# Optimization experiments

Measured on AMD Instinct MI355X. Metric: run time of the kernel, lower is better.

## Reference

```python
import jax, jax.numpy as jnp
import numpy as np

B, C, D, H = 16, 64, 512, 8
SEQ_LEN, LABEL_LEN, PRED_LEN = 1024, 512, 512
DEC_LEN = LABEL_LEN + PRED_LEN
DFF, KSIZE, FACTOR = 2048, 25, 3
E_LAYERS, D_LAYERS = 2, 1


def _pos_emb(L, d):
    pos = np.arange(L, dtype=np.float32)[:, None]
    div = np.exp(np.arange(0, d, 2, dtype=np.float32) * (-np.log(10000.0) / d))
    pe = np.zeros((L, d), np.float32)
    pe[:, 0::2] = np.sin(pos * div)
    pe[:, 1::2] = np.cos(pos * div)
    return jnp.asarray(pe)


def moving_mean(x, k=KSIZE):
    # AvgPool1d(k, stride=1) with replicate padding of (k-1)//2 at both ends
    pad = (k - 1) // 2
    xp = jnp.concatenate([jnp.repeat(x[:, :1], pad, 1), x, jnp.repeat(x[:, -1:], pad, 1)], axis=1)
    cs = jnp.cumsum(xp, axis=1)
    cs = jnp.concatenate([jnp.zeros_like(cs[:, :1]), cs], axis=1)
    return (cs[:, k:] - cs[:, :-k]) / k


def series_decomp(x):
    mm = moving_mean(x)
    return x - mm, mm


def circ_conv3(x, W):
    # Conv1d kernel=3, circular padding=1, no bias. x [B,L,Cin], W [3,Cin,Cout]
    L = x.shape[1]
    xp = jnp.concatenate([x[:, -1:], x, x[:, :1]], axis=1)
    return sum(jnp.einsum('blc,cd->bld', xp[:, k:k + L], W[k]) for k in range(3))


def my_layernorm(x, g, b):
    # LayerNorm then subtract per-sample mean over the time axis (special seasonal layernorm)
    mu = x.mean(-1, keepdims=True)
    var = x.var(-1, keepdims=True)
    xh = (x - mu) / jnp.sqrt(var + 1e-5) * g + b
    return xh - xh.mean(axis=1, keepdims=True)


def autocorrelation(q, k, v):
    # q,k,v: [B,L,H,E]. FFT cross-correlation, top-k lag selection, time-delay aggregation.
    L = q.shape[1]
    qf = jnp.fft.rfft(q.transpose(0, 2, 3, 1), axis=-1)
    kf = jnp.fft.rfft(k.transpose(0, 2, 3, 1), axis=-1)
    corr = jnp.fft.irfft(qf * jnp.conj(kf), n=L, axis=-1)  # [B,H,E,L]
    top_k = int(FACTOR * np.log(L))
    w, delay = jax.lax.top_k(corr.mean(axis=(1, 2)), top_k)  # [B,K]
    tc = jax.nn.softmax(w, axis=-1)
    vp = v.transpose(0, 2, 3, 1)  # [B,H,E,L]
    base = jnp.arange(L)
    agg = jnp.zeros_like(vp)
    for i in range(top_k):  # small fixed K (= int(factor*log L) = 20)
        idx = (base[None, :] + delay[:, i:i + 1]) % L  # circular shift == gather on doubled values
        pattern = jnp.take_along_axis(vp, idx[:, None, None, :], axis=-1)
        agg = agg + pattern * tc[:, i][:, None, None, None]
    return agg.transpose(0, 3, 1, 2)  # [B,L,H,E]


def ac_layer(q_in, kv_in, Wq, bq, Wk, bk, Wv, bv, Wo, bo):
    Bb, L, _ = q_in.shape
    S = kv_in.shape[1]
    E = D // H
    q = (q_in @ Wq + bq).reshape(Bb, L, H, E)
    k = (kv_in @ Wk + bk).reshape(Bb, S, H, E)
    v = (kv_in @ Wv + bv).reshape(Bb, S, H, E)
    out = autocorrelation(q, k, v)  # L == S by construction here
    return out.reshape(Bb, L, D) @ Wo + bo


def _forward(x_enc, x_dec, enc_emb_w, dec_emb_w, enc_Wq, enc_bq, enc_Wk, enc_bk, enc_Wv, enc_bv, enc_Wo, enc_bo, enc_ff1, enc_ff2, enc_ng, enc_nb, dsa_Wq, dsa_bq, dsa_Wk, dsa_bk, dsa_Wv, dsa_bv, dsa_Wo, dsa_bo, dca_Wq, dca_bq, dca_Wk, dca_bk, dca_Wv, dca_bv, dca_Wo, dca_bo, dec_ff1, dec_ff2, dec_trend_w, proj_w, proj_b):
    mean = jnp.repeat(x_enc.mean(axis=1, keepdims=True), PRED_LEN, axis=1)
    zeros = jnp.zeros((x_dec.shape[0], PRED_LEN, x_dec.shape[2]), x_enc.dtype)
    seasonal_init, trend_init = series_decomp(x_enc)
    trend = jnp.concatenate([trend_init[:, -LABEL_LEN:], mean], axis=1)
    seasonal_init = jnp.concatenate([seasonal_init[:, -LABEL_LEN:], zeros], axis=1)
    # encoder (DataEmbedding_wo_temp = token circular conv + sinusoidal pos, dropout=0)
    x = circ_conv3(x_enc, enc_emb_w) + _pos_emb(SEQ_LEN, D)[None]
    for l in range(E_LAYERS):
        x = x + ac_layer(x, x, enc_Wq[l], enc_bq[l], enc_Wk[l], enc_bk[l], enc_Wv[l], enc_bv[l], enc_Wo[l], enc_bo[l])
        x, _ = series_decomp(x)
        y = jax.nn.gelu(x @ enc_ff1[l], approximate=False) @ enc_ff2[l]
        x, _ = series_decomp(x + y)
    enc_out = my_layernorm(x, enc_ng, enc_nb)
    # decoder
    xd = circ_conv3(seasonal_init, dec_emb_w) + _pos_emb(DEC_LEN, D)[None]
    for l in range(D_LAYERS):
        xd = xd + ac_layer(xd, xd, dsa_Wq[l], dsa_bq[l], dsa_Wk[l], dsa_bk[l], dsa_Wv[l], dsa_bv[l], dsa_Wo[l], dsa_bo[l])
        xd, t1 = series_decomp(xd)
        xd = xd + ac_layer(xd, enc_out, dca_Wq[l], dca_bq[l], dca_Wk[l], dca_bk[l], dca_Wv[l], dca_bv[l], dca_Wo[l], dca_bo[l])
        xd, t2 = series_decomp(xd)
        y = jax.nn.gelu(xd @ dec_ff1[l], approximate=False) @ dec_ff2[l]
        xd, t3 = series_decomp(xd + y)
        trend = trend + circ_conv3(t1 + t2 + t3, dec_trend_w[l])  # trend projection conv
    seasonal = xd @ proj_w + proj_b
    out = trend + seasonal
    return out[:, -PRED_LEN:]


def setup_inputs():
    key = jax.random.key(0)
    ks = iter(jax.random.split(key, 64))
    def n(shape, s=0.02):
        return jax.random.normal(next(ks), shape, jnp.float32) * s
    inp = {}
    inp['x_enc'] = jax.random.normal(next(ks), (B, SEQ_LEN, C), jnp.float32)
    inp['x_dec'] = jax.random.normal(next(ks), (B, DEC_LEN, C), jnp.float32)
    inp['enc_emb_w'] = n((3, C, D))
    inp['dec_emb_w'] = n((3, C, D))
    for p in ['Wq', 'Wk', 'Wv', 'Wo']:
        bp = p.replace('W', 'b')
        inp['enc_' + p] = n((E_LAYERS, D, D)); inp['enc_' + bp] = jnp.zeros((E_LAYERS, D))
        inp['dsa_' + p] = n((D_LAYERS, D, D)); inp['dsa_' + bp] = jnp.zeros((D_LAYERS, D))
        inp['dca_' + p] = n((D_LAYERS, D, D)); inp['dca_' + bp] = jnp.zeros((D_LAYERS, D))
    inp['enc_ff1'] = n((E_LAYERS, D, DFF)); inp['enc_ff2'] = n((E_LAYERS, DFF, D))
    inp['enc_ng'] = jnp.ones((D,), jnp.float32); inp['enc_nb'] = jnp.zeros((D,), jnp.float32)
    inp['dec_ff1'] = n((D_LAYERS, D, DFF)); inp['dec_ff2'] = n((D_LAYERS, DFF, D))
    inp['dec_trend_w'] = n((D_LAYERS, 3, D, C))
    inp['proj_w'] = n((D, C)); inp['proj_b'] = jnp.zeros((C,), jnp.float32)
    return inp


def reference(x_enc, x_dec, enc_emb_w, dec_emb_w, enc_Wq, enc_bq, enc_Wk, enc_bk, enc_Wv, enc_bv, enc_Wo, enc_bo, enc_ff1, enc_ff2, enc_ng, enc_nb, dsa_Wq, dsa_bq, dsa_Wk, dsa_bk, dsa_Wv, dsa_bv, dsa_Wo, dsa_bo, dca_Wq, dca_bq, dca_Wk, dca_bk, dca_Wv, dca_bv, dca_Wo, dca_bo, dec_ff1, dec_ff2, dec_trend_w, proj_w, proj_b):
    return _forward(x_enc, x_dec, enc_emb_w, dec_emb_w, enc_Wq, enc_bq, enc_Wk, enc_bk, enc_Wv, enc_bv, enc_Wo, enc_bo, enc_ff1, enc_ff2, enc_ng, enc_nb, dsa_Wq, dsa_bq, dsa_Wk, dsa_bk, dsa_Wv, dsa_bv, dsa_Wo, dsa_bo, dca_Wq, dca_bq, dca_Wk, dca_bk, dca_Wv, dca_bv, dca_Wo, dca_bo, dec_ff1, dec_ff2, dec_trend_w, proj_w, proj_b)
```

## Files before the change

kernel.cpp:

```cpp
#include <hip/hip_runtime.h>
#include <math.h>

#define B_   16
#define L_   1024
#define C_   64
#define D_   512
#define DFF_ 2048
#define TOPK_ 20

typedef float f4 __attribute__((ext_vector_type(4)));
typedef float f32x4 __attribute__((ext_vector_type(4)));
typedef short bf16x8 __attribute__((ext_vector_type(8)));
typedef unsigned short u16x8 __attribute__((ext_vector_type(8)));

__device__ __forceinline__ unsigned short f2bf(float f) {
    union { float f; unsigned u; } a; a.f = f;
    unsigned r = a.u + 0x7fff + ((a.u >> 16) & 1);
    return (unsigned short)(r >> 16);
}
__device__ __forceinline__ float bf2f(unsigned short h) {
    union { unsigned u; float f; } a; a.u = ((unsigned)h) << 16;
    return a.f;
}

__device__ __forceinline__ float gelu_fast(float c) {
    float z  = c * 0.70710678118654752f;
    float az = fabsf(z);
    float t  = __builtin_amdgcn_rcpf(fmaf(0.3275911f, az, 1.0f));
    float p  = fmaf(fmaf(fmaf(fmaf(1.061405429f, t, -1.453152027f), t,
                              1.421413741f), t, -0.284496736f), t, 0.254829592f) * t;
    float e  = __expf(-z * z);
    float ea = fmaf(-p, e, 1.0f);
    float er = copysignf(ea, z);
    return 0.5f * c * (1.0f + er);
}

__device__ __forceinline__ void gld16(const void* g, void* l) {
    __builtin_amdgcn_global_load_lds(
        (const __attribute__((address_space(1))) unsigned int*)g,
        (__attribute__((address_space(3))) unsigned int*)l, 16, 0, 0);
}


__global__ __launch_bounds__(256)
void gemm_bf16(const unsigned short* __restrict__ A, const unsigned short* __restrict__ Bt,
               float* __restrict__ Cf, unsigned short* __restrict__ Cb,
               unsigned short* __restrict__ Cl,
               const float* __restrict__ bias, int M, int N, int K, int flags, int nx)
{
    __shared__ unsigned short As0[128 * 32], As1[128 * 32];
    __shared__ unsigned short Bs0[128 * 32], Bs1[128 * 32];
    const int tid = threadIdx.x;
    const int wave = tid >> 6, lane = tid & 63;

    int total = gridDim.x;
    int h = blockIdx.x;
    int lidx = h;
    if ((total & 7) == 0) {
        int q = total >> 3;
        lidx = (h & 7) * q + (h >> 3);
    }
    const int bm = (lidx / nx) * 128, bn = (lidx % nx) * 128;
    const int wm = (wave >> 1) << 6, wn = (wave & 1) << 6;

    const int r0 = (wave << 5) + (lane >> 2);
    const int kq = (((lane & 3) ^ ((lane >> 3) & 3)) << 3);
    const unsigned short* Ap0 = A + (size_t)(bm + r0) * K + kq;
    const unsigned short* Ap1 = Ap0 + (size_t)16 * K;
    const unsigned short* Bp0 = Bt + (size_t)(bn + r0) * K + kq;
    const unsigned short* Bp1 = Bp0 + (size_t)16 * K;
    const int wo0 = (wave << 5) * 32, wo1 = ((wave << 5) + 16) * 32;

    const int la = lane & 15, h4 = lane >> 4;
    const int sw = (la >> 1) & 3;
    f32x4 acc[4][4] = {};

    for (int k0 = 0; k0 < K; k0 += 64) {
        gld16(Ap0 + k0, &As0[wo0]);      gld16(Ap1 + k0, &As0[wo1]);
        gld16(Bp0 + k0, &Bs0[wo0]);      gld16(Bp1 + k0, &Bs0[wo1]);
        gld16(Ap0 + k0 + 32, &As1[wo0]); gld16(Ap1 + k0 + 32, &As1[wo1]);
        gld16(Bp0 + k0 + 32, &Bs1[wo0]); gld16(Bp1 + k0 + 32, &Bs1[wo1]);
        __syncthreads();
        bf16x8 a[4], b[4];
#pragma unroll
        for (int i = 0; i < 4; ++i) {
            a[i] = *(const bf16x8*)&As0[(wm + i * 16 + la) * 32 + ((h4 ^ sw) << 3)];
            b[i] = *(const bf16x8*)&Bs0[(wn + i * 16 + la) * 32 + ((h4 ^ sw) << 3)];
        }
#pragma unroll
        for (int mi = 0; mi < 4; ++mi)
#pragma unroll
            for (int ni = 0; ni < 4; ++ni)
                acc[mi][ni] = __builtin_amdgcn_mfma_f32_16x16x32_bf16(a[mi], b[ni], acc[mi][ni], 0, 0, 0);
#pragma unroll
        for (int i = 0; i < 4; ++i) {
            a[i] = *(const bf16x8*)&As1[(wm + i * 16 + la) * 32 + ((h4 ^ sw) << 3)];
            b[i] = *(const bf16x8*)&Bs1[(wn + i * 16 + la) * 32 + ((h4 ^ sw) << 3)];
        }
#pragma unroll
        for (int mi = 0; mi < 4; ++mi)
#pragma unroll
            for (int ni = 0; ni < 4; ++ni)
                acc[mi][ni] = __builtin_amdgcn_mfma_f32_16x16x32_bf16(a[mi], b[ni], acc[mi][ni], 0, 0, 0);
        __syncthreads();
    }

#pragma unroll
    for (int mi = 0; mi < 4; ++mi) {
#pragma unroll
        for (int r = 0; r < 4; ++r) {
            int m = bm + wm + mi * 16 + h4 * 4 + r;
#pragma unroll
            for (int ni = 0; ni < 4; ++ni) {
                int n = bn + wn + ni * 16 + la;
                float c = acc[mi][ni][r];
                if (bias) c += bias[n];
                if (flags & 2) c = gelu_fast(c);
                size_t o = (size_t)m * N + n;
                if (Cf) { if (flags & 1) Cf[o] += c; else Cf[o] = c; }
                if (Cb) {
                    unsigned short hb = f2bf(c);
                    Cb[o] = hb;
                    if (Cl) Cl[o] = f2bf(c - bf2f(hb));
                }
            }
        }
    }
}

__global__ __launch_bounds__(512)
void gemm256_gelu(const unsigned short* __restrict__ A, const unsigned short* __restrict__ Bt,
                  unsigned short* __restrict__ Cb, int M, int N, int K, int nx)
{
    __shared__ unsigned short As[2][16384];
    __shared__ unsigned short Bs[2][16384];
    const int tid = threadIdx.x;
    const int wave = tid >> 6, lane = tid & 63;

    int total = gridDim.x;
    int h = blockIdx.x;
    int lidx = h;
    if ((total & 7) == 0) {
        int q = total >> 3;
        lidx = (h & 7) * q + (h >> 3);
    }
    const int bm = (lidx / nx) * 256, bn = (lidx % nx) * 256;
    const int wm = (wave >> 2) << 7, wn = (wave & 3) << 6;

    const int r0 = (wave << 5) + (lane >> 2);
    const int kq = (((lane & 3) ^ ((lane >> 3) & 3)) << 3);
    const unsigned short* Ap0 = A + (size_t)(bm + r0) * K + kq;
    const unsigned short* Ap1 = Ap0 + (size_t)16 * K;
    const unsigned short* Bp0 = Bt + (size_t)(bn + r0) * K + kq;
    const unsigned short* Bp1 = Bp0 + (size_t)16 * K;
    const int wo0 = (wave << 5) * 32, wo1 = ((wave << 5) + 16) * 32;

    const int la = lane & 15, h4 = lane >> 4;
    const int sw = (la >> 1) & 3;
    f32x4 acc[8][4] = {};

    gld16(Ap0, &As[0][wo0]);             gld16(Ap1, &As[0][wo1]);
    gld16(Bp0, &Bs[0][wo0]);             gld16(Bp1, &Bs[0][wo1]);
    gld16(Ap0 + 32, &As[0][8192 + wo0]); gld16(Ap1 + 32, &As[0][8192 + wo1]);
    gld16(Bp0 + 32, &Bs[0][8192 + wo0]); gld16(Bp1 + 32, &Bs[0][8192 + wo1]);
    __syncthreads();

    const int nt = K >> 6;
    for (int t = 0; t < nt; ++t) {
        if (t + 1 < nt) {
            const int k0 = (t + 1) << 6;
            const int nb2 = (t + 1) & 1;
            gld16(Ap0 + k0, &As[nb2][wo0]);             gld16(Ap1 + k0, &As[nb2][wo1]);
            gld16(Bp0 + k0, &Bs[nb2][wo0]);             gld16(Bp1 + k0, &Bs[nb2][wo1]);
            gld16(Ap0 + k0 + 32, &As[nb2][8192 + wo0]); gld16(Ap1 + k0 + 32, &As[nb2][8192 + wo1]);
            gld16(Bp0 + k0 + 32, &Bs[nb2][8192 + wo0]); gld16(Bp1 + k0 + 32, &Bs[nb2][8192 + wo1]);
        }
        const int cb = t & 1;
#pragma unroll
        for (int hh = 0; hh < 2; ++hh) {
            const int hb = hh << 13;
            bf16x8 a[8], b[4];
#pragma unroll
            for (int i = 0; i < 8; ++i)
                a[i] = *(const bf16x8*)&As[cb][hb + (wm + i * 16 + la) * 32 + ((h4 ^ sw) << 3)];
#pragma unroll
            for (int i = 0; i < 4; ++i)
                b[i] = *(const bf16x8*)&Bs[cb][hb + (wn + i * 16 + la) * 32 + ((h4 ^ sw) << 3)];
#pragma unroll
            for (int mi = 0; mi < 8; ++mi)
#pragma unroll
                for (int ni = 0; ni < 4; ++ni)
                    acc[mi][ni] = __builtin_amdgcn_mfma_f32_16x16x32_bf16(a[mi], b[ni], acc[mi][ni], 0, 0, 0);
        }
        __syncthreads();
    }

#pragma unroll
    for (int mi = 0; mi < 8; ++mi)
#pragma unroll
        for (int r = 0; r < 4; ++r) {
            int m = bm + wm + mi * 16 + h4 * 4 + r;
#pragma unroll
            for (int ni = 0; ni < 4; ++ni) {
                int n = bn + wn + ni * 16 + la;
                Cb[(size_t)m * N + n] = f2bf(gelu_fast(acc[mi][ni][r]));
            }
        }
}

__global__ __launch_bounds__(256)
void gemm_split(const unsigned short* __restrict__ A, const unsigned short* __restrict__ Bt,
                unsigned short* __restrict__ o0h, unsigned short* __restrict__ o0l, const float* __restrict__ b0,
                unsigned short* __restrict__ o1h, unsigned short* __restrict__ o1l, const float* __restrict__ b1,
                unsigned short* __restrict__ o2h, unsigned short* __restrict__ o2l, const float* __restrict__ b2,
                float* __restrict__ Gz, int M, int N, int K, int nx)
{
    __shared__ unsigned short As0[128 * 32], As1[128 * 32];
    __shared__ unsigned short Bs0[128 * 32], Bs1[128 * 32];
    const int tid = threadIdx.x;
    const int wave = tid >> 6, lane = tid & 63;

    int total = gridDim.x;
    int h = blockIdx.x;
    if (Gz && h < 64) Gz[h * 256 + tid] = 0.f;
    int lidx = h;
    if ((total & 7) == 0) {
        int q = total >> 3;
        lidx = (h & 7) * q + (h >> 3);
    }
    const int bm = (lidx / nx) * 128, bn = (lidx % nx) * 128;
    const int wm = (wave >> 1) << 6, wn = (wave & 1) << 6;

    const int sel = bn >> 9;
    unsigned short* oh = sel == 0 ? o0h : (sel == 1 ? o1h : o2h);
    unsigned short* ol = sel == 0 ? o0l : (sel == 1 ? o1l : o2l);
    const float* bias  = sel == 0 ? b0  : (sel == 1 ? b1  : b2);
    const int nb = bn & 511;

    const int r0 = (wave << 5) + (lane >> 2);
    const int kq = (((lane & 3) ^ ((lane >> 3) & 3)) << 3);
    const unsigned short* Ap0 = A + (size_t)(bm + r0) * K + kq;
    const unsigned short* Ap1 = Ap0 + (size_t)16 * K;
    const unsigned short* Bp0 = Bt + (size_t)(bn + r0) * K + kq;
    const unsigned short* Bp1 = Bp0 + (size_t)16 * K;
    const int wo0 = (wave << 5) * 32, wo1 = ((wave << 5) + 16) * 32;

    const int la = lane & 15, h4 = lane >> 4;
    const int sw = (la >> 1) & 3;
    f32x4 acc[4][4] = {};

    for (int k0 = 0; k0 < K; k0 += 64) {
        gld16(Ap0 + k0, &As0[wo0]);      gld16(Ap1 + k0, &As0[wo1]);
        gld16(Bp0 + k0, &Bs0[wo0]);      gld16(Bp1 + k0, &Bs0[wo1]);
        gld16(Ap0 + k0 + 32, &As1[wo0]); gld16(Ap1 + k0 + 32, &As1[wo1]);
        gld16(Bp0 + k0 + 32, &Bs1[wo0]); gld16(Bp1 + k0 + 32, &Bs1[wo1]);
        __syncthreads();
        bf16x8 a[4], b[4];
#pragma unroll
        for (int i = 0; i < 4; ++i) {
            a[i] = *(const bf16x8*)&As0[(wm + i * 16 + la) * 32 + ((h4 ^ sw) << 3)];
            b[i] = *(const bf16x8*)&Bs0[(wn + i * 16 + la) * 32 + ((h4 ^ sw) << 3)];
        }
#pragma unroll
        for (int mi = 0; mi < 4; ++mi)
#pragma unroll
            for (int ni = 0; ni < 4; ++ni)
                acc[mi][ni] = __builtin_amdgcn_mfma_f32_16x16x32_bf16(a[mi], b[ni], acc[mi][ni], 0, 0, 0);
#pragma unroll
        for (int i = 0; i < 4; ++i) {
            a[i] = *(const bf16x8*)&As1[(wm + i * 16 + la) * 32 + ((h4 ^ sw) << 3)];
            b[i] = *(const bf16x8*)&Bs1[(wn + i * 16 + la) * 32 + ((h4 ^ sw) << 3)];
        }
#pragma unroll
        for (int mi = 0; mi < 4; ++mi)
#pragma unroll
            for (int ni = 0; ni < 4; ++ni)
                acc[mi][ni] = __builtin_amdgcn_mfma_f32_16x16x32_bf16(a[mi], b[ni], acc[mi][ni], 0, 0, 0);
        __syncthreads();
    }

#pragma unroll
    for (int mi = 0; mi < 4; ++mi) {
#pragma unroll
        for (int r = 0; r < 4; ++r) {
            int m = bm + wm + mi * 16 + h4 * 4 + r;
#pragma unroll
            for (int ni = 0; ni < 4; ++ni) {
                int n2 = nb + wn + ni * 16 + la;
                float c = acc[mi][ni][r] + bias[n2];
                size_t o = (size_t)m * 512 + n2;
                unsigned short hb = f2bf(c);
                oh[o] = hb;
                if (ol) ol[o] = f2bf(c - bf2f(hb));
            }
        }
    }
}

__global__ __launch_bounds__(256)
void tcast_kernel(const float* __restrict__ W, unsigned short* __restrict__ Wt, int R, int Cc)
{
    __shared__ float t[32][33];
    int bx = blockIdx.x * 32, by = blockIdx.y * 32;
    int tx = threadIdx.x & 31, ty = threadIdx.x >> 5;
#pragma unroll
    for (int i = 0; i < 32; i += 8)
        t[ty + i][tx] = W[(size_t)(by + ty + i) * Cc + bx + tx];
    __syncthreads();
#pragma unroll
    for (int i = 0; i < 32; i += 8)
        Wt[(size_t)(bx + ty + i) * R + by + tx] = f2bf(t[tx][ty + i]);
}

struct P16 { const float* p[16]; };
__global__ __launch_bounds__(256)
void tcast_all(P16 srcs, unsigned short* __restrict__ dst)
{
    __shared__ float t[32][33];
    const float* W = srcs.p[blockIdx.z];
    unsigned short* Wt = dst + (size_t)blockIdx.z * 262144;
    int bx = blockIdx.x * 32, by = blockIdx.y * 32;
    int tx = threadIdx.x & 31, ty = threadIdx.x >> 5;
#pragma unroll
    for (int i = 0; i < 32; i += 8)
        t[ty + i][tx] = W[(size_t)(by + ty + i) * 512 + bx + tx];
    __syncthreads();
#pragma unroll
    for (int i = 0; i < 32; i += 8)
        Wt[(size_t)(bx + ty + i) * 512 + by + tx] = f2bf(t[tx][ty + i]);
}

__global__ __launch_bounds__(256)
void pegen_kernel(float* __restrict__ PE)
{
    int idx = blockIdx.x * blockDim.x + threadIdx.x;
    int n = idx & 511, l = idx >> 9;
    int i2 = n & ~1;
    float div = expf(-(float)i2 * 0.017988946039015984f);
    float ang = (float)l * div;
    PE[idx] = (n & 1) ? cosf(ang) : sinf(ang);
}

__global__ __launch_bounds__(256)
void emb_kernel(const float* __restrict__ A, const float* __restrict__ W,
                const float* __restrict__ PEt,
                float* __restrict__ Xo, unsigned short* __restrict__ Xb)
{
    __shared__ float As[66][68];
    __shared__ float Ws[3][64][64];
    const int tid = threadIdx.x;
    const int bn = blockIdx.x * 64, bm = blockIdx.y * 64;
    const int base = bm & ~1023;
    for (int i = tid; i < 66 * 64; i += 256) {
        int r = i >> 6, c = i & 63;
        int l = (bm - base) + r - 1;
        if (l < 0) l += 1024; else if (l >= 1024) l -= 1024;
        As[r][c] = A[(size_t)(base + l) * 64 + c];
    }
    for (int i = tid; i < 3 * 64 * 64; i += 256) {
        int tap = i >> 12, rem = i & 4095, k = rem >> 6, c = rem & 63;
        Ws[tap][k][c] = W[((size_t)tap * 64 + k) * 512 + bn + c];
    }
    __syncthreads();
    const int tx = tid & 15, ty = tid >> 4;
    float acc[4][4] = {};
    for (int tap = 0; tap < 3; ++tap)
        for (int k = 0; k < 64; ++k) {
            f4 bv = *(const f4*)&Ws[tap][k][tx * 4];
#pragma unroll
            for (int i = 0; i < 4; ++i) {
                float a = As[ty * 4 + i + tap][k];
#pragma unroll
                for (int j = 0; j < 4; ++j)
                    acc[i][j] = fmaf(a, bv[j], acc[i][j]);
            }
        }
#pragma unroll
    for (int i = 0; i < 4; ++i) {
        int m = bm + ty * 4 + i;
        int l = m & 1023;
#pragma unroll
        for (int j = 0; j < 4; ++j) {
            int n = bn + tx * 4 + j;
            float c = acc[i][j] + PEt[((size_t)l << 9) + n];
            size_t o = (size_t)m * 512 + n;
            Xo[o] = c;
            Xb[o] = f2bf(c);
        }
    }
}

__global__ __launch_bounds__(256)
void tail_kernel(const float* __restrict__ TSUM, const float* __restrict__ T1,
                 const float* __restrict__ Wt, const float* __restrict__ pw,
                 float* __restrict__ PC, float* __restrict__ PP)
{
    __shared__ float Ts[18][17];
    __shared__ float T1s[16][17];
    __shared__ float Ws[3][16][64];
    __shared__ float Ps[16][64];
    const int tid = threadIdx.x;
    const int bo = blockIdx.x * 16;
    const int kc = blockIdx.y;
    const int b = bo >> 9;
    const int lbase = (bo & 511) + 512;
    const size_t rowbase = (size_t)b << 10;
    const int tc4 = (tid & 15) * 4;
    const int tr = tid >> 4;
    const int kbeg = kc * 64, kend = kbeg + 64;
    float cacc[4] = {}, pacc[4] = {};

    for (int k0 = kbeg; k0 < kend; k0 += 16) {
        for (int i = tid; i < 18 * 16; i += 256) {
            int r = i >> 4, c = i & 15;
            int l = lbase + r - 1; if (l >= 1024) l -= 1024;
            Ts[r][c] = TSUM[(rowbase + l) * 512 + k0 + c];
        }
        {
            int r = tid >> 4, c = tid & 15;
            T1s[r][c] = T1[(rowbase + lbase + r) * 512 + k0 + c];
        }
        for (int i = tid; i < 3 * 16 * 16; i += 256) {
            int tap = i / 256, rem = i & 255, k = rem >> 4, c4 = (rem & 15) * 4;
            *(f4*)&Ws[tap][k][c4] = *(const f4*)&Wt[((size_t)tap * 512 + k0 + k) * 64 + c4];
        }
        if (tid < 256) {
            int k = tid >> 4, c4 = (tid & 15) * 4;
            *(f4*)&Ps[k][c4] = *(const f4*)&pw[(size_t)(k0 + k) * 64 + c4];
        }
        __syncthreads();
        for (int tap = 0; tap < 3; ++tap)
#pragma unroll
            for (int k = 0; k < 16; ++k) {
                f4 bv = *(const f4*)&Ws[tap][k][tc4];
                float a = Ts[tr + tap][k];
#pragma unroll
                for (int j = 0; j < 4; ++j)
                    cacc[j] = fmaf(a, bv[j], cacc[j]);
            }
#pragma unroll
        for (int k = 0; k < 16; ++k) {
            f4 bv = *(const f4*)&Ps[k][tc4];
            float a = T1s[tr][k];
#pragma unroll
            for (int j = 0; j < 4; ++j)
                pacc[j] = fmaf(a, bv[j], pacc[j]);
        }
        __syncthreads();
    }
    size_t o = ((size_t)kc * 8192 + (bo + tr)) * 64 + tc4;
    *(f4*)&PC[o] = *(f4*)cacc;
    *(f4*)&PP[o] = *(f4*)pacc;
}

__global__ __launch_bounds__(256)
void tailred_kernel(const float* __restrict__ PC, const float* __restrict__ PP,
                    const float* __restrict__ MEANC, const float* __restrict__ pb,
                    float* __restrict__ OUT)
{
    int idx = blockIdx.x * blockDim.x + threadIdx.x;
    int n = idx & 63;
    int b = idx >> 15;
    const size_t S = (size_t)8192 * 64;
    float cs = PC[idx];
    float ps = PP[idx];
#pragma unroll
    for (int s = 1; s < 8; ++s) {
        cs += PC[s * S + idx];
        ps += PP[s * S + idx];
    }
    OUT[idx] = (MEANC[(b << 6) + n] + cs) + (ps + pb[n]);
}

__global__ __launch_bounds__(512)
void corr_mfma(const unsigned short* __restrict__ Qh, const unsigned short* __restrict__ Ql,
               const unsigned short* __restrict__ Kh, const unsigned short* __restrict__ Kl,
               float* __restrict__ G)
{
    __shared__ unsigned short Qhs[2][8192], Qls[2][8192], Khs[2][8192], Kls[2][8192];
    __shared__ float diagw[8][512];
    const int tid = threadIdx.x;
    const int wave = tid >> 6, lane = tid & 63;

    const int i_ = blockIdx.x;
    const int x_ = i_ & 7, j_ = i_ >> 3;
    const int b = x_ + ((j_ >> 4) << 3);
    const int tile = j_ & 15;
    const int bt = (tile >> 2) * 256, bs = (tile & 3) * 256;

    const int wm = (wave >> 2) << 7, wn = (wave & 3) << 6;
    const size_t boff = (size_t)b << 19;

    const int r0 = (wave << 5) + (lane >> 2);
    const int kq = (((lane & 3) ^ ((lane >> 3) & 3)) << 3);
    const size_t g0 = boff + (size_t)(bt + r0) * 512 + kq;
    const size_t g1 = g0 + (size_t)16 * 512;
    const size_t p0 = boff + (size_t)(bs + r0) * 512 + kq;
    const size_t p1 = p0 + (size_t)16 * 512;
    const int wo0 = (wave << 5) * 32, wo1 = ((wave << 5) + 16) * 32;

    {
        float* dz = &diagw[0][0];
#pragma unroll
        for (int i = 0; i < 8; ++i) dz[tid + i * 512] = 0.f;
    }

    const int la = lane & 15, h4 = lane >> 4;
    const int sw = (la >> 1) & 3;
    f32x4 acc[8][4] = {};

    gld16(Qh + g0, &Qhs[0][wo0]); gld16(Qh + g1, &Qhs[0][wo1]);
    gld16(Ql + g0, &Qls[0][wo0]); gld16(Ql + g1, &Qls[0][wo1]);
    gld16(Kh + p0, &Khs[0][wo0]); gld16(Kh + p1, &Khs[0][wo1]);
    gld16(Kl + p0, &Kls[0][wo0]); gld16(Kl + p1, &Kls[0][wo1]);
    __syncthreads();

    for (int t = 0; t < 16; ++t) {
        if (t + 1 < 16) {
            const int k0 = (t + 1) << 5;
            const int nb2 = (t + 1) & 1;
            gld16(Qh + g0 + k0, &Qhs[nb2][wo0]); gld16(Qh + g1 + k0, &Qhs[nb2][wo1]);
            gld16(Ql + g0 + k0, &Qls[nb2][wo0]); gld16(Ql + g1 + k0, &Qls[nb2][wo1]);
            gld16(Kh + p0 + k0, &Khs[nb2][wo0]); gld16(Kh + p1 + k0, &Khs[nb2][wo1]);
            gld16(Kl + p0 + k0, &Kls[nb2][wo0]); gld16(Kl + p1 + k0, &Kls[nb2][wo1]);
        }
        const int cb = t & 1;
        bf16x8 ah[8], bh[4];
#pragma unroll
        for (int i = 0; i < 8; ++i)
            ah[i] = *(const bf16x8*)&Qhs[cb][(wm + i * 16 + la) * 32 + ((h4 ^ sw) << 3)];
#pragma unroll
        for (int i = 0; i < 4; ++i)
            bh[i] = *(const bf16x8*)&Khs[cb][(wn + i * 16 + la) * 32 + ((h4 ^ sw) << 3)];
#pragma unroll
        for (int mi = 0; mi < 8; ++mi)
#pragma unroll
            for (int ni = 0; ni < 4; ++ni)
                acc[mi][ni] = __builtin_amdgcn_mfma_f32_16x16x32_bf16(ah[mi], bh[ni], acc[mi][ni], 0, 0, 0);
        {
            bf16x8 bl[4];
#pragma unroll
            for (int i = 0; i < 4; ++i)
                bl[i] = *(const bf16x8*)&Kls[cb][(wn + i * 16 + la) * 32 + ((h4 ^ sw) << 3)];
#pragma unroll
            for (int mi = 0; mi < 8; ++mi)
#pragma unroll
                for (int ni = 0; ni < 4; ++ni)
                    acc[mi][ni] = __builtin_amdgcn_mfma_f32_16x16x32_bf16(ah[mi], bl[ni], acc[mi][ni], 0, 0, 0);
        }
        {
            bf16x8 al[8];
#pragma unroll
            for (int i = 0; i < 8; ++i)
                al[i] = *(const bf16x8*)&Qls[cb][(wm + i * 16 + la) * 32 + ((h4 ^ sw) << 3)];
#pragma unroll
            for (int mi = 0; mi < 8; ++mi)
#pragma unroll
                for (int ni = 0; ni < 4; ++ni)
                    acc[mi][ni] = __builtin_amdgcn_mfma_f32_16x16x32_bf16(al[mi], bh[ni], acc[mi][ni], 0, 0, 0);
        }
        __syncthreads();
    }

    float rbin[11][4] = {};
#pragma unroll
    for (int mi = 0; mi < 8; ++mi)
#pragma unroll
        for (int ni = 0; ni < 4; ++ni)
#pragma unroll
            for (int r = 0; r < 4; ++r)
                rbin[mi - ni + 3][r] += acc[mi][ni][r];

    const int base = (wm - wn) + 4 * h4 - la + 255;
#pragma unroll
    for (int d = 0; d < 11; ++d)
#pragma unroll
        for (int r = 0; r < 4; ++r)
            atomicAdd(&diagw[wave][base + 16 * (d - 3) + r], rbin[d][r]);
    __syncthreads();
    if (tid < 511) {
        float s = 0.f;
#pragma unroll
        for (int w = 0; w < 8; ++w) s += diagw[w][tid];
        int n = (bt - bs + tid - 255) & 1023;
        atomicAdd(&G[(b << 10) + n], s);
    }
}

__global__ __launch_bounds__(256)
void topk_kernel(const float* __restrict__ G, int* __restrict__ delay,
                 float* __restrict__ tc)
{
    __shared__ float vals[1024];
    __shared__ float pw[4];
    __shared__ int   pwi[4];
    __shared__ float wsel[TOPK_];
    __shared__ int   isel[TOPK_];
    const int b = blockIdx.x, tid = threadIdx.x;
    const int lane = tid & 63, wid = tid >> 6;
    for (int i = tid; i < 1024; i += 256) vals[i] = G[(b << 10) + i] * (1.0f / 512.0f);
    __syncthreads();
    for (int it = 0; it < TOPK_; ++it) {
        float bv = -INFINITY; int bi = 0;
#pragma unroll
        for (int u = 0; u < 4; ++u) {
            int i = tid * 4 + u;
            float v = vals[i];
            if (v > bv) { bv = v; bi = i; }
        }
#pragma unroll
        for (int o = 32; o > 0; o >>= 1) {
            float ov = __shfl_xor(bv, o, 64);
            int   oi = __shfl_xor(bi, o, 64);
            if (ov > bv || (ov == bv && oi < bi)) { bv = ov; bi = oi; }
        }
        if (lane == 0) { pw[wid] = bv; pwi[wid] = bi; }
        __syncthreads();
        if (tid == 0) {
            float m = pw[0]; int mi = pwi[0];
#pragma unroll
            for (int t = 1; t < 4; ++t)
                if (pw[t] > m || (pw[t] == m && pwi[t] < mi)) { m = pw[t]; mi = pwi[t]; }
            wsel[it] = m; isel[it] = mi;
            vals[mi] = -INFINITY;
        }
        __syncthreads();
    }
    if (tid == 0) {
        float m = wsel[0];
#pragma unroll
        for (int i = 1; i < TOPK_; ++i) m = fmaxf(m, wsel[i]);
        float e[TOPK_], s = 0.f;
#pragma unroll
        for (int i = 0; i < TOPK_; ++i) { e[i] = expf(wsel[i] - m); s += e[i]; }
        float inv = 1.0f / s;
#pragma unroll
        for (int i = 0; i < TOPK_; ++i) {
            tc[b * TOPK_ + i] = e[i] * inv;
            delay[b * TOPK_ + i] = isel[i];
        }
    }
}

__global__ __launch_bounds__(256)
void agg_kernel(const unsigned short* __restrict__ V, const int* __restrict__ delay,
                const float* __restrict__ tc, unsigned short* __restrict__ out)
{
    __shared__ int   dls[TOPK_];
    __shared__ float tcs[TOPK_];
    int h = blockIdx.x, g = gridDim.x, lh = h;
    if ((g & 7) == 0) {
        int q = g >> 3;
        lh = (h & 7) * q + (h >> 3);
    }
    int idx = (lh * blockDim.x + threadIdx.x) * 8;
    int d = idx & 511;
    int l = (idx >> 9) & 1023;
    int b = idx >> 19;
    if (threadIdx.x < TOPK_) {
        dls[threadIdx.x] = delay[b * TOPK_ + threadIdx.x];
        tcs[threadIdx.x] = tc[b * TOPK_ + threadIdx.x];
    }
    __syncthreads();
    const unsigned short* Vb = V + ((size_t)b << 19);
    float s[8] = {};
#pragma unroll
    for (int i = 0; i < TOPK_; ++i) {
        int row = (l + dls[i]) & 1023;
        float w = tcs[i];
        u16x8 v = *(const u16x8*)&Vb[((size_t)row << 9) + d];
#pragma unroll
        for (int j = 0; j < 8; ++j)
            s[j] = fmaf(w, bf2f(v[j]), s[j]);
    }
    u16x8 o;
#pragma unroll
    for (int j = 0; j < 8; ++j) o[j] = f2bf(s[j]);
    *(u16x8*)&out[idx] = o;
}

__global__ void decomp_kernel(const float* __restrict__ x, float* __restrict__ seas,
                              unsigned short* __restrict__ seasb,
                              float* __restrict__ trend, int Bn, int Ln, int Ch,
                              int nseg, int tmode)
{
    int h = blockIdx.x, g = gridDim.x, lh = h;
    if ((g & 7) == 0) {
        int q = g >> 3;
        lh = (h & 7) * q + (h >> 3);
    }
    int idx = lh * blockDim.x + threadIdx.x;
    int total = Bn * Ch * nseg;
    if (idx >= total) return;
    int ch = idx % Ch;
    int rest = idx / Ch;
    int seg = rest % nseg;
    int b = rest / nseg;
    int segL = Ln / nseg;
    int l0 = seg * segL;
    const float* xp = x + (size_t)b * Ln * Ch + ch;
    float* sp = seas + (size_t)b * Ln * Ch + ch;
    unsigned short* bp = seasb ? seasb + (size_t)b * Ln * Ch + ch : nullptr;
    float* tp = trend ? trend + (size_t)b * Ln * Ch + ch : nullptr;
    float s = 0.f;
    for (int j = -12; j <= 12; ++j) {
        int t = l0 + j;
        t = t < 0 ? 0 : (t > Ln - 1 ? Ln - 1 : t);
        s += xp[(size_t)t * Ch];
    }
    for (int l = l0; l < l0 + segL; ++l) {
        float mm = s * (1.0f / 25.0f);
        float v = xp[(size_t)l * Ch] - mm;
        sp[(size_t)l * Ch] = v;
        if (bp) bp[(size_t)l * Ch] = f2bf(v);
        if (tmode == 1) tp[(size_t)l * Ch] = mm;
        else if (tmode == 2) tp[(size_t)l * Ch] += mm;
        int ta = l + 13; if (ta > Ln - 1) ta = Ln - 1;
        int ts = l - 12; if (ts < 0) ts = 0;
        s += xp[(size_t)ta * Ch] - xp[(size_t)ts * Ch];
    }
}

__global__ __launch_bounds__(256)
void lnrow_kernel(const float* __restrict__ x, const float* __restrict__ g,
                  const float* __restrict__ bv, float* __restrict__ out)
{
    __shared__ float sh1[4], sh2[4];
    int row = blockIdx.x, tid = threadIdx.x;
    const float* xr = x + ((size_t)row << 9);
    float v0 = xr[tid], v1 = xr[tid + 256];
    float s = v0 + v1, q = v0 * v0 + v1 * v1;
#pragma unroll
    for (int o = 32; o > 0; o >>= 1) {
        s += __shfl_down(s, o, 64);
        q += __shfl_down(q, o, 64);
    }
    int wid = tid >> 6;
    if ((tid & 63) == 0) { sh1[wid] = s; sh2[wid] = q; }
    __syncthreads();
    if (tid == 0) {
        sh1[0] = sh1[0] + sh1[1] + sh1[2] + sh1[3];
        sh2[0] = sh2[0] + sh2[1] + sh2[2] + sh2[3];
    }
    __syncthreads();
    float mu = sh1[0] * (1.0f / 512.0f);
    float var = sh2[0] * (1.0f / 512.0f) - mu * mu;
    float inv = rsqrtf(var + 1e-5f);
    out[((size_t)row << 9) + tid] = (v0 - mu) * inv * g[tid] + bv[tid];
    out[((size_t)row << 9) + tid + 256] = (v1 - mu) * inv * g[tid + 256] + bv[tid + 256];
}

__global__ void colmean_kernel(const float* __restrict__ x, float* __restrict__ m)
{
    int idx = blockIdx.x * blockDim.x + threadIdx.x;
    if (idx >= B_ * D_) return;
    int b = idx >> 9, d = idx & 511;
    const float* xp = x + ((size_t)b << 19) + d;
    float s = 0.f;
    for (int l = 0; l < L_; ++l) s += xp[(size_t)l << 9];
    m[idx] = s * (1.0f / 1024.0f);
}

__global__ void colsub_kernel(const float* __restrict__ x, const float* __restrict__ m,
                              unsigned short* __restrict__ out)
{
    int idx = blockIdx.x * blockDim.x + threadIdx.x;
    int d = idx & 511;
    int b = idx >> 19;
    out[idx] = f2bf(x[idx] - m[(b << 9) + d]);
}

__global__ void meanx_kernel(const float* __restrict__ x, float* __restrict__ m)
{
    int idx = blockIdx.x * blockDim.x + threadIdx.x;
    if (idx >= B_ * C_) return;
    int b = idx >> 6, c = idx & 63;
    const float* xp = x + (size_t)b * L_ * C_ + c;
    float s = 0.f;
    for (int l = 0; l < L_; ++l) s += xp[(size_t)l << 6];
    m[idx] = s * (1.0f / 1024.0f);
}

__global__ void builddec_kernel(const float* __restrict__ seenc, float* __restrict__ seasin)
{
    int idx = blockIdx.x * blockDim.x + threadIdx.x;
    int c = idx & 63;
    int l = (idx >> 6) & 1023;
    int b = idx >> 16;
    if (l < 512) {
        int src = (b << 16) + ((512 + l) << 6) + c;
        seasin[idx] = seenc[src];
    } else {
        seasin[idx] = 0.f;
    }
}

extern "C" void kernel_launch(void* const* d_in, const int* in_sizes, int n_in,
                              void* d_out, int out_size, void* d_ws, size_t ws_size,
                              hipStream_t stream)
{
    auto F = [&](int i) { return (const float*)d_in[i]; };
    const float* x_enc     = F(0);
    const float* enc_emb_w = F(2);
    const float* dec_emb_w = F(3);
    const float* enc_Wq = F(4);  const float* enc_bq = F(5);
    const float* dsa_Wq = F(6);  const float* dsa_bq = F(7);
    const float* dca_Wq = F(8);  const float* dca_bq = F(9);
    const float* enc_Wk = F(10); const float* enc_bk = F(11);
    const float* dsa_Wk = F(12); const float* dsa_bk = F(13);
    const float* dca_Wk = F(14); const float* dca_bk = F(15);
    const float* enc_Wv = F(16); const float* enc_bv = F(17);
    const float* dsa_Wv = F(18); const float* dsa_bv = F(19);
    const float* dca_Wv = F(20); const float* dca_bv = F(21);
    const float* enc_Wo = F(22); const float* enc_bo = F(23);
    const float* dsa_Wo = F(24); const float* dsa_bo = F(25);
    const float* dca_Wo = F(26); const float* dca_bo = F(27);
    const float* enc_ff1 = F(28); const float* enc_ff2 = F(29);
    const float* enc_ng = F(30);  const float* enc_nb = F(31);
    const float* dec_ff1 = F(32); const float* dec_ff2 = F(33);
    const float* dec_trend_w = F(34);
    const float* proj_w = F(35);  const float* proj_b = F(36);

    constexpr size_t F512 = (size_t)B_ * L_ * D_;
    constexpr size_t F64  = (size_t)B_ * L_ * C_;
    constexpr size_t SMALL = 1024 + 16384 + 320 + 320 + 8192;
    constexpr size_t WTSA_N = 16 * 262144;
    constexpr size_t WTSF_N = 2 * 1024 * 1024;
    size_t need = (3 * F512 + 2 * F64 + SMALL) * 4 + (8 * F512 + WTSA_N + WTSF_N) * 2;
    if (ws_size < need) return;

    float* X      = (float*)d_ws;
    float* T1     = X + F512;
    float* TSUM   = T1 + F512;
    float* SEASIN = TSUM + F512;
    float* PET    = SEASIN + F64;
    float* MEANC  = PET + F64;
    float* G      = MEANC + 1024;
    float* TCW    = G + 16384;
    int*   DEL    = (int*)(TCW + 320);
    float* LNMEAN = (float*)(DEL + 320);
    unsigned short* AB   = (unsigned short*)(LNMEAN + 8192);
    unsigned short* EB   = AB + F512;
    unsigned short* VB   = EB + F512;
    unsigned short* HB   = VB + F512;
    unsigned short* QHI  = HB + F512;
    unsigned short* QLO  = QHI + F512;
    unsigned short* KHI  = QLO + F512;
    unsigned short* KLO  = KHI + F512;
    unsigned short* WTSA = KLO + F512;
    unsigned short* WTSF = WTSA + WTSA_N;
    float* OUT = (float*)d_out;

    const int M = B_ * L_;

    auto mgemm = [&](const unsigned short* A, const unsigned short* Bt, float* Cf,
                     unsigned short* Cb, unsigned short* Cl, const float* bias,
                     int Mm, int Nn, int Kk, int flags) {
        int nx = Nn / 128;
        int total = nx * (Mm / 128);
        gemm_bf16<<<total, 256, 0, stream>>>(A, Bt, Cf, Cb, Cl, bias, Mm, Nn, Kk, flags, nx);
    };
    auto tcast = [&](const float* W, unsigned short* Wt, int R, int Cc) {
        tcast_kernel<<<dim3(Cc / 32, R / 32), 256, 0, stream>>>(W, Wt, R, Cc);
    };
    auto corr_topk_agg = [&]() {
        corr_mfma<<<256, 512, 0, stream>>>(QHI, QLO, KHI, KLO, G);
        topk_kernel<<<16, 256, 0, stream>>>(G, DEL, TCW);
        agg_kernel<<<(int)(F512 / 8 / 256), 256, 0, stream>>>(VB, DEL, TCW, HB);
    };
    auto attn_self = [&](const unsigned short* xin, int slotbase,
                         const float* bq, const float* bk, const float* bvp, const float* bo,
                         float* resid) {
        gemm_split<<<12 * 128, 256, 0, stream>>>(xin, WTSA + (size_t)slotbase * 262144,
            QHI, QLO, bq, KHI, KLO, bk, VB, nullptr, bvp, G, M, 1536, 512, 12);
        corr_topk_agg();
        mgemm(HB, WTSA + (size_t)(slotbase + 3) * 262144, resid, nullptr, nullptr, bo, M, 512, 512, 1);
    };
    auto attn_cross = [&](const unsigned short* qin, const unsigned short* kvin, int slotbase,
                          const float* bq, const float* bk, const float* bvp, const float* bo,
                          float* resid) {
        mgemm(qin, WTSA + (size_t)slotbase * 262144, nullptr, QHI, QLO, bq, M, 512, 512, 0);
        gemm_split<<<8 * 128, 256, 0, stream>>>(kvin, WTSA + (size_t)(slotbase + 1) * 262144,
            KHI, KLO, bk, VB, nullptr, bvp, nullptr, nullptr, nullptr, G, M, 1024, 512, 8);
        corr_topk_agg();
        mgemm(HB, WTSA + (size_t)(slotbase + 3) * 262144, resid, nullptr, nullptr, bo, M, 512, 512, 1);
    };
    auto ffblock = [&](const unsigned short* xin, const float* W1, const float* W2, float* resid) {
        unsigned short* Wf1 = WTSF;
        unsigned short* Wf2 = WTSF + 1048576;
        unsigned short* HFULL = QHI;
        tcast(W1, Wf1, 512, 2048);
        tcast(W2, Wf2, 2048, 512);
        gemm256_gelu<<<512, 512, 0, stream>>>(xin, Wf1, HFULL, M, 2048, 512, 8);
        mgemm(HFULL, Wf2, resid, nullptr, nullptr, nullptr, M, 512, 2048, 1);
    };

    {
        P16 srcs;
        for (int l = 0; l < 2; ++l) {
            srcs.p[l * 4 + 0] = enc_Wq + (size_t)l * 262144;
            srcs.p[l * 4 + 1] = enc_Wk + (size_t)l * 262144;
            srcs.p[l * 4 + 2] = enc_Wv + (size_t)l * 262144;
            srcs.p[l * 4 + 3] = enc_Wo + (size_t)l * 262144;
        }
        srcs.p[8]  = dsa_Wq; srcs.p[9]  = dsa_Wk; srcs.p[10] = dsa_Wv; srcs.p[11] = dsa_Wo;
        srcs.p[12] = dca_Wq; srcs.p[13] = dca_Wk; srcs.p[14] = dca_Wv; srcs.p[15] = dca_Wo;
        tcast_all<<<dim3(16, 16, 16), 256, 0, stream>>>(srcs, WTSA);
    }
    pegen_kernel<<<2048, 256, 0, stream>>>(PET);

    float* SEENC = (float*)QHI;
    decomp_kernel<<<(B_ * C_ * 64 + 255) / 256, 256, 0, stream>>>(x_enc, SEENC, nullptr, nullptr, B_, L_, C_, 64, 0);
    meanx_kernel<<<(B_ * C_ + 255) / 256, 256, 0, stream>>>(x_enc, MEANC);
    builddec_kernel<<<(int)(F64 / 256), 256, 0, stream>>>(SEENC, SEASIN);

    emb_kernel<<<dim3(8, 256), 256, 0, stream>>>(x_enc, enc_emb_w, PET, X, AB);

    for (int l = 0; l < 2; ++l) {
        attn_self(AB, l * 4,
                  enc_bq + l * D_, enc_bk + l * D_, enc_bv + l * D_, enc_bo + l * D_, X);
        decomp_kernel<<<(B_ * D_ * 64 + 255) / 256, 256, 0, stream>>>(X, T1, AB, nullptr, B_, L_, D_, 64, 0);
        ffblock(AB, enc_ff1 + (size_t)l * D_ * DFF_, enc_ff2 + (size_t)l * DFF_ * D_, T1);
        decomp_kernel<<<(B_ * D_ * 64 + 255) / 256, 256, 0, stream>>>(T1, X, AB, nullptr, B_, L_, D_, 64, 0);
    }
    lnrow_kernel<<<M, 256, 0, stream>>>(X, enc_ng, enc_nb, T1);
    colmean_kernel<<<(B_ * D_ + 255) / 256, 256, 0, stream>>>(T1, LNMEAN);
    colsub_kernel<<<(int)(F512 / 256), 256, 0, stream>>>(T1, LNMEAN, EB);

    float* XD = X;
    emb_kernel<<<dim3(8, 256), 256, 0, stream>>>(SEASIN, dec_emb_w, PET, XD, AB);

    attn_self(AB, 8, dsa_bq, dsa_bk, dsa_bv, dsa_bo, XD);
    decomp_kernel<<<(B_ * D_ * 64 + 255) / 256, 256, 0, stream>>>(XD, T1, AB, TSUM, B_, L_, D_, 64, 1);

    attn_cross(AB, EB, 12, dca_bq, dca_bk, dca_bv, dca_bo, T1);
    decomp_kernel<<<(B_ * D_ * 64 + 255) / 256, 256, 0, stream>>>(T1, XD, AB, TSUM, B_, L_, D_, 64, 2);

    ffblock(AB, dec_ff1, dec_ff2, XD);
    decomp_kernel<<<(B_ * D_ * 64 + 255) / 256, 256, 0, stream>>>(XD, T1, nullptr, TSUM, B_, L_, D_, 64, 2);

    float* PART_C = (float*)QHI;
    float* PART_P = PART_C + (size_t)8 * 8192 * 64;
    tail_kernel<<<dim3(512, 8), 256, 0, stream>>>(TSUM, T1, dec_trend_w, proj_w, PART_C, PART_P);
    tailred_kernel<<<2048, 256, 0, stream>>>(PART_C, PART_P, MEANC, proj_b, OUT);
}
```

Baseline: 1.676 ms.

## Enlarge QKV split GEMM tile to 256x256 with double-buffered LDS prefetch

The fused QKV/KV projection GEMM now uses 256x256 output tiles with 512 threads (8 waves, each computing 128x64) instead of 128x128 tiles with 256 threads. The next K-slice is loaded asynchronously into a second LDS buffer while the current one is consumed, removing the load-then-wait stall of the old loop. The larger tile raises data reuse per LDS load but uses 128KB of LDS per block and more accumulator registers. It also launches far fewer blocks (384 or 256), which can leave CUs unevenly loaded.

```diff
diff --git a/kernel.cpp b/kernel.cpp
--- a/kernel.cpp
+++ b/kernel.cpp
@@ -208,28 +208,28 @@
         }
 }
 
-__global__ __launch_bounds__(256)
-void gemm_split(const unsigned short* __restrict__ A, const unsigned short* __restrict__ Bt,
-                unsigned short* __restrict__ o0h, unsigned short* __restrict__ o0l, const float* __restrict__ b0,
-                unsigned short* __restrict__ o1h, unsigned short* __restrict__ o1l, const float* __restrict__ b1,
-                unsigned short* __restrict__ o2h, unsigned short* __restrict__ o2l, const float* __restrict__ b2,
-                float* __restrict__ Gz, int M, int N, int K, int nx)
-{
-    __shared__ unsigned short As0[128 * 32], As1[128 * 32];
-    __shared__ unsigned short Bs0[128 * 32], Bs1[128 * 32];
+__global__ __launch_bounds__(512)
+void gemm_split256(const unsigned short* __restrict__ A, const unsigned short* __restrict__ Bt,
+                   unsigned short* __restrict__ o0h, unsigned short* __restrict__ o0l, const float* __restrict__ b0,
+                   unsigned short* __restrict__ o1h, unsigned short* __restrict__ o1l, const float* __restrict__ b1,
+                   unsigned short* __restrict__ o2h, unsigned short* __restrict__ o2l, const float* __restrict__ b2,
+                   float* __restrict__ Gz, int M, int N, int K, int nx)
+{
+    __shared__ unsigned short As[2][16384];
+    __shared__ unsigned short Bs[2][16384];
     const int tid = threadIdx.x;
     const int wave = tid >> 6, lane = tid & 63;
 
     int total = gridDim.x;
     int h = blockIdx.x;
-    if (Gz && h < 64) Gz[h * 256 + tid] = 0.f;
+    if (Gz && h < 32) Gz[h * 512 + tid] = 0.f;
     int lidx = h;
     if ((total & 7) == 0) {
         int q = total >> 3;
         lidx = (h & 7) * q + (h >> 3);
     }
-    const int bm = (lidx / nx) * 128, bn = (lidx % nx) * 128;
-    const int wm = (wave >> 1) << 6, wn = (wave & 1) << 6;
+    const int bm = (lidx / nx) * 256, bn = (lidx % nx) * 256;
+    const int wm = (wave >> 2) << 7, wn = (wave & 3) << 6;
 
     const int sel = bn >> 9;
     unsigned short* oh = sel == 0 ? o0h : (sel == 1 ? o1h : o2h);
@@ -247,40 +247,46 @@
 
     const int la = lane & 15, h4 = lane >> 4;
     const int sw = (la >> 1) & 3;
-    f32x4 acc[4][4] = {};
-
-    for (int k0 = 0; k0 < K; k0 += 64) {
-        gld16(Ap0 + k0, &As0[wo0]);      gld16(Ap1 + k0, &As0[wo1]);
-        gld16(Bp0 + k0, &Bs0[wo0]);      gld16(Bp1 + k0, &Bs0[wo1]);
-        gld16(Ap0 + k0 + 32, &As1[wo0]); gld16(Ap1 + k0 + 32, &As1[wo1]);
-        gld16(Bp0 + k0 + 32, &Bs1[wo0]); gld16(Bp1 + k0 + 32, &Bs1[wo1]);
+    f32x4 acc[8][4] = {};
+
+    gld16(Ap0, &As[0][wo0]);             gld16(Ap1, &As[0][wo1]);
+    gld16(Bp0, &Bs[0][wo0]);             gld16(Bp1, &Bs[0][wo1]);
+    gld16(Ap0 + 32, &As[0][8192 + wo0]); gld16(Ap1 + 32, &As[0][8192 + wo1]);
+    gld16(Bp0 + 32, &Bs[0][8192 + wo0]); gld16(Bp1 + 32, &Bs[0][8192 + wo1]);
+    __syncthreads();
+
+    const int nt = K >> 6;
+    for (int t = 0; t < nt; ++t) {
+        if (t + 1 < nt) {
+            const int k0 = (t + 1) << 6;
+            const int nb2 = (t + 1) & 1;
+            gld16(Ap0 + k0, &As[nb2][wo0]);             gld16(Ap1 + k0, &As[nb2][wo1]);
+            gld16(Bp0 + k0, &Bs[nb2][wo0]);             gld16(Bp1 + k0, &Bs[nb2][wo1]);
+            gld16(Ap0 + k0 + 32, &As[nb2][8192 + wo0]); gld16(Ap1 + k0 + 32, &As[nb2][8192 + wo1]);
+            gld16(Bp0 + k0 + 32, &Bs[nb2][8192 + wo0]); gld16(Bp1 + k0 + 32, &Bs[nb2][8192 + wo1]);
+        }
+        const int cb = t & 1;
+#pragma unroll
+        for (int hh = 0; hh < 2; ++hh) {
+            const int hb = hh << 13;
+            bf16x8 a[8], b[4];
+#pragma unroll
+            for (int i = 0; i < 8; ++i)
+                a[i] = *(const bf16x8*)&As[cb][hb + (wm + i * 16 + la) * 32 + ((h4 ^ sw) << 3)];
+#pragma unroll
+            for (int i = 0; i < 4; ++i)
+                b[i] = *(const bf16x8*)&Bs[cb][hb + (wn + i * 16 + la) * 32 + ((h4 ^ sw) << 3)];
+#pragma unroll
+            for (int mi = 0; mi < 8; ++mi)
+#pragma unroll
+                for (int ni = 0; ni < 4; ++ni)
+                    acc[mi][ni] = __builtin_amdgcn_mfma_f32_16x16x32_bf16(a[mi], b[ni], acc[mi][ni], 0, 0, 0);
+        }
         __syncthreads();
-        bf16x8 a[4], b[4];
-#pragma unroll
-        for (int i = 0; i < 4; ++i) {
-            a[i] = *(const bf16x8*)&As0[(wm + i * 16 + la) * 32 + ((h4 ^ sw) << 3)];
-            b[i] = *(const bf16x8*)&Bs0[(wn + i * 16 + la) * 32 + ((h4 ^ sw) << 3)];
-        }
-#pragma unroll
-        for (int mi = 0; mi < 4; ++mi)
-#pragma unroll
-            for (int ni = 0; ni < 4; ++ni)
-                acc[mi][ni] = __builtin_amdgcn_mfma_f32_16x16x32_bf16(a[mi], b[ni], acc[mi][ni], 0, 0, 0);
-#pragma unroll
-        for (int i = 0; i < 4; ++i) {
-            a[i] = *(const bf16x8*)&As1[(wm + i * 16 + la) * 32 + ((h4 ^ sw) << 3)];
-            b[i] = *(const bf16x8*)&Bs1[(wn + i * 16 + la) * 32 + ((h4 ^ sw) << 3)];
-        }
-#pragma unroll
-        for (int mi = 0; mi < 4; ++mi)
-#pragma unroll
-            for (int ni = 0; ni < 4; ++ni)
-                acc[mi][ni] = __builtin_amdgcn_mfma_f32_16x16x32_bf16(a[mi], b[ni], acc[mi][ni], 0, 0, 0);
-        __syncthreads();
-    }
-
-#pragma unroll
-    for (int mi = 0; mi < 4; ++mi) {
+    }
+
+#pragma unroll
+    for (int mi = 0; mi < 8; ++mi)
 #pragma unroll
         for (int r = 0; r < 4; ++r) {
             int m = bm + wm + mi * 16 + h4 * 4 + r;
@@ -289,12 +295,11 @@
                 int n2 = nb + wn + ni * 16 + la;
                 float c = acc[mi][ni][r] + bias[n2];
                 size_t o = (size_t)m * 512 + n2;
-                unsigned short hb = f2bf(c);
-                oh[o] = hb;
-                if (ol) ol[o] = f2bf(c - bf2f(hb));
+                unsigned short hb2 = f2bf(c);
+                oh[o] = hb2;
+                if (ol) ol[o] = f2bf(c - bf2f(hb2));
             }
         }
-    }
 }
 
 __global__ __launch_bounds__(256)
@@ -871,8 +876,8 @@
     auto attn_self = [&](const unsigned short* xin, int slotbase,
                          const float* bq, const float* bk, const float* bvp, const float* bo,
                          float* resid) {
-        gemm_split<<<12 * 128, 256, 0, stream>>>(xin, WTSA + (size_t)slotbase * 262144,
-            QHI, QLO, bq, KHI, KLO, bk, VB, nullptr, bvp, G, M, 1536, 512, 12);
+        gemm_split256<<<6 * 64, 512, 0, stream>>>(xin, WTSA + (size_t)slotbase * 262144,
+            QHI, QLO, bq, KHI, KLO, bk, VB, nullptr, bvp, G, M, 1536, 512, 6);
         corr_topk_agg();
         mgemm(HB, WTSA + (size_t)(slotbase + 3) * 262144, resid, nullptr, nullptr, bo, M, 512, 512, 1);
     };
@@ -880,8 +885,8 @@
                           const float* bq, const float* bk, const float* bvp, const float* bo,
                           float* resid) {
         mgemm(qin, WTSA + (size_t)slotbase * 262144, nullptr, QHI, QLO, bq, M, 512, 512, 0);
-        gemm_split<<<8 * 128, 256, 0, stream>>>(kvin, WTSA + (size_t)(slotbase + 1) * 262144,
-            KHI, KLO, bk, VB, nullptr, bvp, nullptr, nullptr, nullptr, G, M, 1024, 512, 8);
+        gemm_split256<<<4 * 64, 512, 0, stream>>>(kvin, WTSA + (size_t)(slotbase + 1) * 262144,
+            KHI, KLO, bk, VB, nullptr, bvp, nullptr, nullptr, nullptr, G, M, 1024, 512, 4);
         corr_topk_agg();
         mgemm(HB, WTSA + (size_t)(slotbase + 3) * 262144, resid, nullptr, nullptr, bo, M, 512, 512, 1);
     };
```

Result: no change. 1.682 ms (+0.4%).
